# Kernel optimization log

Hardware: AMD Instinct MI355X
Metric: run time of the kernel (lower is better)

## Reference

```python
import jax, jax.numpy as jnp
import numpy as np
import math

B, D, S, H = 4, 1024, 2048, 16


def setup_inputs() -> dict:
    key = jax.random.key(0)
    ks = jax.random.split(key, 9)
    scale = 0.02
    return {
        "x": jax.random.normal(ks[0], (B, D, S), dtype=jnp.float32),
        "Wq": jax.random.normal(ks[1], (D, D), dtype=jnp.float32) * scale,
        "bq": jnp.zeros((D,), dtype=jnp.float32),
        "Wk": jax.random.normal(ks[2], (D, D), dtype=jnp.float32) * scale,
        "bk": jnp.zeros((D,), dtype=jnp.float32),
        "Wv": jax.random.normal(ks[3], (D, D), dtype=jnp.float32) * scale,
        "bv": jnp.zeros((D,), dtype=jnp.float32),
        "Wo": jax.random.normal(ks[4], (D, D), dtype=jnp.float32) * scale,
        "bo": jnp.zeros((D,), dtype=jnp.float32),
        "num_heads": H,
    }


def _positional_encoding(d_model, seq_len):
    # pe[0::2, :] = sin(pos * denom), pe[1::2, :] = cos(pos * denom)
    pos = jnp.arange(seq_len, dtype=jnp.float32)[None, :]            # [1, S]
    denom = jnp.exp(jnp.arange(0, d_model, 2, dtype=jnp.float32)
                    * (-math.log(10000.0) / d_model))[:, None]        # [D/2, 1]
    angles = pos * denom                                              # [D/2, S]
    pe = jnp.zeros((d_model, seq_len), dtype=jnp.float32)
    pe = pe.at[0::2, :].set(jnp.sin(angles))
    pe = pe.at[1::2, :].set(jnp.cos(angles))
    return pe


def reference(x, Wq, bq, Wk, bk, Wv, bv, Wo, bo, num_heads):
    b, d_model, s = x.shape
    head_dim = d_model // num_heads
    x = x + _positional_encoding(d_model, s)[None, :, :]  # broadcast over batch
    x = jnp.transpose(x, (0, 2, 1))                       # [B, S, D]
    q = x @ Wq.T + bq
    k = x @ Wk.T + bk
    v = x @ Wv.T + bv
    # [B, S, H, hd] -> [B, H, S, hd]
    q = q.reshape(b, s, num_heads, head_dim).transpose(0, 2, 1, 3)
    k = k.reshape(b, s, num_heads, head_dim).transpose(0, 2, 1, 3)
    v = v.reshape(b, s, num_heads, head_dim).transpose(0, 2, 1, 3)
    scores = jnp.einsum('bhqd,bhkd->bhqk', q, k) / jnp.sqrt(
        jnp.asarray(head_dim, dtype=jnp.float32))
    attn = jax.nn.softmax(scores, axis=-1)
    out = jnp.einsum('bhqk,bhkd->bhqd', attn, v)          # [B, H, S, hd]
    out = out.transpose(0, 2, 1, 3).reshape(b, s, d_model)
    out = out @ Wo.T + bo
    return jnp.transpose(out, (0, 2, 1))                  # [B, D, S]
```

## Files before the change

kernel.cpp:

```cpp
#include <hip/hip_runtime.h>


typedef __bf16 bf16;
typedef __attribute__((ext_vector_type(8))) __bf16 bf16x8;
typedef __attribute__((ext_vector_type(4))) __bf16 bf16x4;
typedef __attribute__((ext_vector_type(2))) __bf16 bf16x2;
typedef __attribute__((ext_vector_type(4))) float f32x4;
typedef __attribute__((ext_vector_type(2))) unsigned int uintx2;
typedef __attribute__((ext_vector_type(4))) unsigned int uintx4;

#define NB 4
#define ND 1024
#define NS 2048
#define NH 16
#define NM 8192

__device__ __forceinline__ void gld16(const void* g, void* l) {
  __builtin_amdgcn_global_load_lds((__attribute__((address_space(1))) void*)g,
                                   (__attribute__((address_space(3))) void*)l, 16, 0, 0);
}

__device__ __forceinline__ float exp2_fast(float x) {
#if __has_builtin(__builtin_amdgcn_exp2f)
  return __builtin_amdgcn_exp2f(x);
#else
  return exp2f(x);
#endif
}

__device__ __forceinline__ unsigned pk2(float a, float b) {
  bf16x2 t;
  t[0] = (bf16)a;
  t[1] = (bf16)b;
  return __builtin_bit_cast(unsigned int, t);
}

__device__ __forceinline__ void lane_xchg(unsigned a, unsigned b, unsigned& lo,
                                          unsigned& hi) {
#if __has_builtin(__builtin_amdgcn_permlane32_swap) && \
    __has_builtin(__builtin_amdgcn_permlane16_swap)
  uintx2 r = __builtin_amdgcn_permlane32_swap(a, b, false, false);
  uintx2 r2 = __builtin_amdgcn_permlane16_swap(r[0], r[1], false, false);
  lo = r2[0];
  hi = r2[1];
#else
  const int lane = threadIdx.x & 63;
  const int src = (lane & 15) + ((lane >> 4) & 1) * 32;
  const unsigned as = (unsigned)__shfl((int)a, src, 64);
  const unsigned bs = (unsigned)__shfl((int)b, src, 64);
  const unsigned as2 = (unsigned)__shfl((int)a, src + 16, 64);
  const unsigned bs2 = (unsigned)__shfl((int)b, src + 16, 64);
  lo = (lane >= 32) ? bs : as;
  hi = (lane >= 32) ? bs2 : as2;
#endif
}

__global__ __launch_bounds__(256) void prep_kernel(
    const float* __restrict__ x, const float* __restrict__ Wq,
    const float* __restrict__ Wk, const float* __restrict__ Wv,
    const float* __restrict__ Wo, bf16* __restrict__ xT, bf16* __restrict__ Wqkv,
    bf16* __restrict__ WoB) {
  const int tx = threadIdx.x, ty = threadIdx.y;
  if (blockIdx.z == NB) {
    const size_t flat = ((size_t)blockIdx.y * 64 + blockIdx.x) * 256 + ty * 32 + tx;
#pragma unroll
    for (int c = 0; c < 2; ++c) {
      const size_t i = (flat * 2 + c) * 4;
      const float* src;
      bf16* dst;
      size_t off;
      if (i < (size_t)3 * 1024 * 1024) {
        const int sel = (int)(i >> 20);
        src = sel == 0 ? Wq : (sel == 1 ? Wk : Wv);
        off = i - ((size_t)sel << 20);
        dst = Wqkv + i;
      } else {
        src = Wo;
        off = i - ((size_t)3 << 20);
        dst = WoB + off;
      }
      const f32x4 v = *(const f32x4*)(src + off);
      bf16x4 o;
      o[0] = (bf16)v[0];
      o[1] = (bf16)v[1];
      o[2] = (bf16)v[2];
      o[3] = (bf16)v[3];
      *(bf16x4*)dst = o;
    }
    return;
  }
  __shared__ float t[32][33];
  const int s0 = blockIdx.x * 32, d0 = blockIdx.y * 32, b = blockIdx.z;
#pragma unroll
  for (int i = 0; i < 4; ++i) {
    const int rr = ty + i * 8;
    const int d = d0 + rr, s = s0 + tx;
    const float freq = __expf(-(float)(d >> 1) * 0.01798894603980689f);
    const float ang = (float)s * freq;
    const float pe = (d & 1) ? __cosf(ang) : __sinf(ang);
    t[rr][tx] = x[((size_t)b * ND + d) * NS + s] + pe;
  }
  __syncthreads();
#pragma unroll
  for (int i = 0; i < 4; ++i) {
    const int a = ty + i * 8;
    xT[((size_t)b * NS + s0 + a) * ND + d0 + tx] = (bf16)t[tx][a];
  }
}

__device__ __forceinline__ void gemm_tile_128(const bf16* __restrict__ A,
                                              const bf16* __restrict__ Bm,
                                              int tm, int tn, bf16* ldsA, bf16* ldsB,
                                              f32x4 acc[4][4]) {
  const int tid = threadIdx.x;
  const int lane = tid & 63, wave = tid >> 6;
  const int wm = wave >> 1, wn = wave & 1;
  const int rl = lane & 15, quad = lane >> 4;
  int r0[4], c0[4];
#pragma unroll
  for (int j = 0; j < 4; ++j) {
    const int o = (wave * 4 + j) * 1024 + lane * 16;
    const int r = o >> 7;
    r0[j] = r;
    c0[j] = ((((o >> 4) & 7) ^ (r & 7)) * 8);
  }
  for (int kt = 0; kt < 1024; kt += 64) {
#pragma unroll
    for (int j = 0; j < 4; ++j) {
      gld16(A + (size_t)(tm + r0[j]) * 1024 + kt + c0[j], (char*)ldsA + (wave * 4 + j) * 1024);
      gld16(Bm + (size_t)(tn + r0[j]) * 1024 + kt + c0[j], (char*)ldsB + (wave * 4 + j) * 1024);
    }
    __syncthreads();
#pragma unroll
    for (int kk = 0; kk < 2; ++kk) {
      bf16x8 af[4], bfr[4];
#pragma unroll
      for (int i = 0; i < 4; ++i) {
        const int ra = wm * 64 + i * 16 + rl;
        af[i] = *(const bf16x8*)((const char*)ldsA + ra * 128 +
                                 (((kk * 4 + quad) ^ (rl & 7)) * 16));
        const int rb = wn * 64 + i * 16 + rl;
        bfr[i] = *(const bf16x8*)((const char*)ldsB + rb * 128 +
                                  (((kk * 4 + quad) ^ (rl & 7)) * 16));
      }
#pragma unroll
      for (int i = 0; i < 4; ++i)
#pragma unroll
        for (int j = 0; j < 4; ++j)
          acc[i][j] =
              __builtin_amdgcn_mfma_f32_16x16x32_bf16(af[i], bfr[j], acc[i][j], 0, 0, 0);
    }
    __syncthreads();
  }
}

__global__ __launch_bounds__(256, 3) void gemm_qkv_kernel(
    const bf16* __restrict__ xT, const bf16* __restrict__ Wqkv,
    const float* __restrict__ bq, const float* __restrict__ bk,
    const float* __restrict__ bv, bf16* __restrict__ Q, bf16* __restrict__ Kb,
    bf16* __restrict__ VT) {
  __shared__ bf16 ldsA[128 * 64], ldsB[128 * 64];
  const int tm = blockIdx.x * 128, tn = blockIdx.y * 128;
  f32x4 acc[4][4];
  const f32x4 z = {0.f, 0.f, 0.f, 0.f};
#pragma unroll
  for (int i = 0; i < 4; ++i)
#pragma unroll
    for (int j = 0; j < 4; ++j) acc[i][j] = z;
  gemm_tile_128(xT, Wqkv, tm, tn, ldsA, ldsB, acc);
  const int lane = threadIdx.x & 63, wave = threadIdx.x >> 6;
  const int wm = wave >> 1, wn = wave & 1;
  const int rl = lane & 15, quad = lane >> 4;
  const float QSCALE = 0.18033688011112042f;
#pragma unroll
  for (int j = 0; j < 4; ++j) {
    const int n = tn + wn * 64 + j * 16 + rl;
    const int which = n >> 10;
    const int nl = n & 1023;
    const int h = nl >> 6, d = nl & 63;
    const float bias = (which == 0 ? bq : which == 1 ? bk : bv)[nl];
#pragma unroll
    for (int i = 0; i < 4; ++i) {
      const int m0 = tm + wm * 64 + i * 16 + quad * 4;
      const int b = m0 >> 11, s0 = m0 & 2047;
      const size_t bh = (size_t)(b * 16 + h);
      if (which == 2) {
        bf16x4 pk;
#pragma unroll
        for (int r = 0; r < 4; ++r) pk[r] = (bf16)(acc[i][j][r] + bias);
        *(bf16x4*)(VT + ((size_t)bh * 64 + d) * 2048 + s0) = pk;
      } else {
#pragma unroll
        for (int r = 0; r < 4; ++r) {
          const float v = acc[i][j][r] + bias;
          const int s = s0 + r;
          if (which == 0)
            Q[(bh * 2048 + s) * 64 + d] = (bf16)(v * QSCALE);
          else
            Kb[(bh * 2048 + s) * 64 + d] = (bf16)v;
        }
      }
    }
  }
}

__global__ __launch_bounds__(256, 4) void attn_kernel(const bf16* __restrict__ Q,
                                                      const bf16* __restrict__ Kb,
                                                      const bf16* __restrict__ VT,
                                                      bf16* __restrict__ AO) {
  __shared__ __align__(16) char smem[32768];
  char* ldsK = smem;
  char* ldsV = smem + 16384;
  const int tid = threadIdx.x;
  const int lane = tid & 63, wave = tid >> 6;
  const int rl = lane & 15, quad = lane >> 4;
  const int bh = blockIdx.x;
  const int q0 = blockIdx.y * 128;
  const bf16* Qb = Q + ((size_t)bh * 2048 + q0) * 64;
  const bf16* Kbb = Kb + (size_t)bh * 2048 * 64;
  const bf16* Vb = VT + (size_t)bh * 64 * 2048;
  const int o0 = wave * 1024 + lane * 16, o1 = o0 + 4096;
  const int ra = o0 >> 7, rb = o1 >> 7;
  const int ca = (((o0 >> 4) & 7) ^ (ra & 7)) * 16;
  const int cb = (((o1 >> 4) & 7) ^ (rb & 7)) * 16;
  gld16((const char*)Kbb + (size_t)ra * 128 + ca, ldsK + wave * 1024);
  gld16((const char*)Kbb + (size_t)rb * 128 + cb, ldsK + wave * 1024 + 4096);
  gld16((const char*)Vb + (size_t)ra * 4096 + ca, ldsV + wave * 1024);
  gld16((const char*)Vb + (size_t)rb * 4096 + cb, ldsV + wave * 1024 + 4096);
  bf16x8 qf[2][2];
#pragma unroll
  for (int i = 0; i < 2; ++i)
#pragma unroll
    for (int ks = 0; ks < 2; ++ks)
      qf[i][ks] =
          *(const bf16x8*)(Qb + (wave * 32 + i * 16 + rl) * 64 + ks * 32 + quad * 8);
  f32x4 o_acc[2][4], lacc[2];
  const f32x4 z = {0.f, 0.f, 0.f, 0.f};
#pragma unroll
  for (int i = 0; i < 2; ++i) {
    lacc[i] = z;
#pragma unroll
    for (int j = 0; j < 4; ++j) o_acc[i][j] = z;
  }
  const bf16 oneb = (bf16)1.0f;
  const bf16x8 onesb = {oneb, oneb, oneb, oneb, oneb, oneb, oneb, oneb};
  int buf = 0;
  for (int kt = 0; kt < 2048; kt += 64, buf ^= 1) {
    __syncthreads();
    if (kt + 64 < 2048) {
      const int nb = (buf ^ 1) * 8192;
      gld16((const char*)Kbb + (size_t)(kt + 64 + ra) * 128 + ca, ldsK + nb + wave * 1024);
      gld16((const char*)Kbb + (size_t)(kt + 64 + rb) * 128 + cb,
            ldsK + nb + wave * 1024 + 4096);
      gld16((const char*)Vb + (size_t)ra * 4096 + (size_t)(kt + 64) * 2 + ca,
            ldsV + nb + wave * 1024);
      gld16((const char*)Vb + (size_t)rb * 4096 + (size_t)(kt + 64) * 2 + cb,
            ldsV + nb + wave * 1024 + 4096);
    }
    const char* Kbase = ldsK + buf * 8192;
    const char* Vbase = ldsV + buf * 8192;
#pragma unroll
    for (int ks = 0; ks < 2; ++ks) {
      const int jk0 = ks * 2, jk1 = ks * 2 + 1;
      const bf16x8 k00 =
          *(const bf16x8*)(Kbase + (jk0 * 16 + rl) * 128 + ((quad ^ (rl & 7)) * 16));
      const bf16x8 k01 =
          *(const bf16x8*)(Kbase + (jk0 * 16 + rl) * 128 + (((4 + quad) ^ (rl & 7)) * 16));
      const bf16x8 k10 =
          *(const bf16x8*)(Kbase + (jk1 * 16 + rl) * 128 + ((quad ^ (rl & 7)) * 16));
      const bf16x8 k11 =
          *(const bf16x8*)(Kbase + (jk1 * 16 + rl) * 128 + (((4 + quad) ^ (rl & 7)) * 16));
      bf16x8 pf[2];
#pragma unroll
      for (int i = 0; i < 2; ++i) {
        f32x4 s0 = z, s1 = z;
        s0 = __builtin_amdgcn_mfma_f32_16x16x32_bf16(k00, qf[i][0], s0, 0, 0, 0);
        s0 = __builtin_amdgcn_mfma_f32_16x16x32_bf16(k01, qf[i][1], s0, 0, 0, 0);
        s1 = __builtin_amdgcn_mfma_f32_16x16x32_bf16(k10, qf[i][0], s1, 0, 0, 0);
        s1 = __builtin_amdgcn_mfma_f32_16x16x32_bf16(k11, qf[i][1], s1, 0, 0, 0);
        const unsigned a0 = pk2(exp2_fast(s0[0]), exp2_fast(s0[1]));
        const unsigned a1 = pk2(exp2_fast(s0[2]), exp2_fast(s0[3]));
        const unsigned b0 = pk2(exp2_fast(s1[0]), exp2_fast(s1[1]));
        const unsigned b1 = pk2(exp2_fast(s1[2]), exp2_fast(s1[3]));
        unsigned d0, d1, d2, d3;
        lane_xchg(a0, b0, d0, d2);
        lane_xchg(a1, b1, d1, d3);
        uintx4 dd;
        dd[0] = d0;
        dd[1] = d1;
        dd[2] = d2;
        dd[3] = d3;
        pf[i] = __builtin_bit_cast(bf16x8, dd);
        lacc[i] =
            __builtin_amdgcn_mfma_f32_16x16x32_bf16(pf[i], onesb, lacc[i], 0, 0, 0);
      }
#pragma unroll
      for (int j = 0; j < 4; ++j) {
        const bf16x8 vf = *(const bf16x8*)(Vbase + (j * 16 + rl) * 128 +
                                           (((ks * 4 + quad) ^ (rl & 7)) * 16));
#pragma unroll
        for (int i = 0; i < 2; ++i)
          o_acc[i][j] =
              __builtin_amdgcn_mfma_f32_16x16x32_bf16(pf[i], vf, o_acc[i][j], 0, 0, 0);
      }
    }
  }
  const int b = bh >> 4, h = bh & 15;
#pragma unroll
  for (int i = 0; i < 2; ++i) {
    f32x4 linv;
#pragma unroll
    for (int r = 0; r < 4; ++r) linv[r] = __builtin_amdgcn_rcpf(lacc[i][r]);
#pragma unroll
    for (int j = 0; j < 4; ++j)
#pragma unroll
      for (int r = 0; r < 4; ++r) {
        const int s = q0 + wave * 32 + i * 16 + quad * 4 + r;
        const int d = h * 64 + j * 16 + rl;
        AO[((size_t)b * 2048 + s) * 1024 + d] = (bf16)(o_acc[i][j][r] * linv[r]);
      }
  }
}

__global__ __launch_bounds__(256, 3) void gemm_out_kernel(const bf16* __restrict__ AO,
                                                          const bf16* __restrict__ WoB,
                                                          const float* __restrict__ bo,
                                                          float* __restrict__ out) {
  __shared__ bf16 ldsA[128 * 64], ldsB[128 * 64];
  const int tm = blockIdx.x * 128, tn = blockIdx.y * 128;
  f32x4 acc[4][4];
  const f32x4 z = {0.f, 0.f, 0.f, 0.f};
#pragma unroll
  for (int i = 0; i < 4; ++i)
#pragma unroll
    for (int j = 0; j < 4; ++j) acc[i][j] = z;
  gemm_tile_128(AO, WoB, tm, tn, ldsA, ldsB, acc);
  const int lane = threadIdx.x & 63, wave = threadIdx.x >> 6;
  const int wm = wave >> 1, wn = wave & 1;
  const int rl = lane & 15, quad = lane >> 4;
#pragma unroll
  for (int j = 0; j < 4; ++j) {
    const int n = tn + wn * 64 + j * 16 + rl;
    const float bias = bo[n];
#pragma unroll
    for (int i = 0; i < 4; ++i) {
      const int m0 = tm + wm * 64 + i * 16 + quad * 4;
      const int b = m0 >> 11, s = m0 & 2047;
      f32x4 v = acc[i][j];
      v[0] += bias;
      v[1] += bias;
      v[2] += bias;
      v[3] += bias;
      *(f32x4*)(out + ((size_t)(b * 1024 + n)) * 2048 + s) = v;
    }
  }
}

extern "C" void kernel_launch(void* const* d_in, const int* in_sizes, int n_in,
                              void* d_out, int out_size, void* d_ws, size_t ws_size,
                              hipStream_t stream) {
  const float* x = (const float*)d_in[0];
  const float* Wq = (const float*)d_in[1];
  const float* bq = (const float*)d_in[2];
  const float* Wk = (const float*)d_in[3];
  const float* bk = (const float*)d_in[4];
  const float* Wv = (const float*)d_in[5];
  const float* bv = (const float*)d_in[6];
  const float* Wo = (const float*)d_in[7];
  const float* bo = (const float*)d_in[8];
  float* out = (float*)d_out;

  char* p = (char*)d_ws;
  bf16* xT = (bf16*)p;
  p += (size_t)NM * ND * 2;
  bf16* Wqkv = (bf16*)p;
  p += (size_t)3 * ND * ND * 2;
  bf16* WoB = (bf16*)p;
  p += (size_t)ND * ND * 2;
  bf16* Qb = (bf16*)p;
  p += (size_t)NM * ND * 2;
  bf16* Kbf = (bf16*)p;
  p += (size_t)NM * ND * 2;
  bf16* VTb = (bf16*)p;
  p += (size_t)NM * ND * 2;
  bf16* AO = xT;

  prep_kernel<<<dim3(NS / 32, ND / 32, NB + 1), dim3(32, 8), 0, stream>>>(
      x, Wq, Wk, Wv, Wo, xT, Wqkv, WoB);
  gemm_qkv_kernel<<<dim3(NM / 128, 3072 / 128), dim3(256), 0, stream>>>(
      xT, Wqkv, bq, bk, bv, Qb, Kbf, VTb);
  attn_kernel<<<dim3(NB * NH, NS / 128), dim3(256), 0, stream>>>(Qb, Kbf, VTb, AO);
  gemm_out_kernel<<<dim3(NM / 128, ND / 128), dim3(256), 0, stream>>>(AO, WoB, bo, out);
}
```

Baseline: 261.2 us.

## Rewrite QKV GEMM with 256x256 tiles, 8 waves and double-buffered LDS prefetch

Replaces the 128x128 QKV projection GEMM with a 512-thread kernel computing 256x256 tiles. It double-buffers 128KB of LDS, issues global-to-LDS loads for the next K-step interleaved with MFMA phases, and uses explicit waitcnt/barriers and setprio. The goal is more data reuse per tile and hiding global load latency behind compute. In exchange, large LDS use limits occupancy, the grid has only 384 blocks, and the hand-placed barriers add fragility. The out-GEMM launch bound also drops from 3 to 2 waves.

Measured after the change: 285.8 us. 1.09x slower.

```diff
diff --git a/kernel.cpp b/kernel.cpp
--- a/kernel.cpp
+++ b/kernel.cpp
@@ -108,6 +108,128 @@
   }
 }
 
+__global__ __launch_bounds__(512, 2) void gemm_qkv_kernel(
+    const bf16* __restrict__ xT, const bf16* __restrict__ Wqkv,
+    const float* __restrict__ bq, const float* __restrict__ bk,
+    const float* __restrict__ bv, bf16* __restrict__ Q, bf16* __restrict__ Kb,
+    bf16* __restrict__ VT) {
+  __shared__ __align__(16) char smem[131072];
+  char* ldsA = smem;
+  char* ldsB = smem + 65536;
+  const int tid = threadIdx.x;
+  const int lane = tid & 63, wave = tid >> 6;
+  const int wm = wave >> 2, wn = wave & 3;
+  const int rl = lane & 15, quad = lane >> 4;
+  const int tm = blockIdx.x * 256, tn = blockIdx.y * 256;
+  int row[4], colv[4];
+#pragma unroll
+  for (int g = 0; g < 4; ++g) {
+    const int c = g * 512 + tid;
+    const int r = c >> 3;
+    row[g] = r;
+    colv[g] = (((c & 7) ^ (r & 7)) * 8);
+  }
+  f32x4 acc[8][4];
+  const f32x4 z = {0.f, 0.f, 0.f, 0.f};
+#pragma unroll
+  for (int i = 0; i < 8; ++i)
+#pragma unroll
+    for (int j = 0; j < 4; ++j) acc[i][j] = z;
+#pragma unroll
+  for (int g = 0; g < 4; ++g) {
+    gld16(xT + (size_t)(tm + row[g]) * 1024 + colv[g], ldsA + g * 8192 + tid * 16);
+    gld16(Wqkv + (size_t)(tn + row[g]) * 1024 + colv[g], ldsB + g * 8192 + tid * 16);
+  }
+  for (int t = 0; t < 16; ++t) {
+    const int cur = t & 1;
+    const char* Ab = ldsA + cur * 32768;
+    const char* Bb = ldsB + cur * 32768;
+    const int nb = (cur ^ 1) * 32768;
+    const int ktn = (t + 1) * 64;
+#pragma unroll
+    for (int p = 0; p < 4; ++p) {
+      if (p == 0) {
+        if (t < 15) {
+          gld16(xT + (size_t)(tm + row[0]) * 1024 + ktn + colv[0],
+                ldsA + nb + tid * 16);
+          gld16(Wqkv + (size_t)(tn + row[0]) * 1024 + ktn + colv[0],
+                ldsB + nb + tid * 16);
+          asm volatile("s_waitcnt vmcnt(2)" ::: "memory");
+        } else {
+          asm volatile("s_waitcnt vmcnt(0)" ::: "memory");
+        }
+        asm volatile("s_barrier" ::: "memory");
+      }
+      const int mq = p >> 1, nq = p & 1;
+      bf16x8 af[4][2], bfr[2][2];
+#pragma unroll
+      for (int i = 0; i < 4; ++i) {
+        const int ra = wm * 128 + mq * 64 + i * 16 + rl;
+#pragma unroll
+        for (int kk = 0; kk < 2; ++kk)
+          af[i][kk] =
+              *(const bf16x8*)(Ab + ra * 128 + (((kk * 4 + quad) ^ (rl & 7)) * 16));
+      }
+#pragma unroll
+      for (int j = 0; j < 2; ++j) {
+        const int rb = wn * 64 + nq * 32 + j * 16 + rl;
+#pragma unroll
+        for (int kk = 0; kk < 2; ++kk)
+          bfr[j][kk] =
+              *(const bf16x8*)(Bb + rb * 128 + (((kk * 4 + quad) ^ (rl & 7)) * 16));
+      }
+      if (p != 0 && t < 15) {
+        gld16(xT + (size_t)(tm + row[p]) * 1024 + ktn + colv[p],
+              ldsA + nb + p * 8192 + tid * 16);
+        gld16(Wqkv + (size_t)(tn + row[p]) * 1024 + ktn + colv[p],
+              ldsB + nb + p * 8192 + tid * 16);
+      }
+      if (p != 0) asm volatile("s_barrier" ::: "memory");
+      __builtin_amdgcn_s_setprio(1);
+#pragma unroll
+      for (int kk = 0; kk < 2; ++kk)
+#pragma unroll
+        for (int i = 0; i < 4; ++i)
+#pragma unroll
+          for (int j = 0; j < 2; ++j)
+            acc[mq * 4 + i][nq * 2 + j] = __builtin_amdgcn_mfma_f32_16x16x32_bf16(
+                af[i][kk], bfr[j][kk], acc[mq * 4 + i][nq * 2 + j], 0, 0, 0);
+      __builtin_amdgcn_s_setprio(0);
+      asm volatile("s_barrier" ::: "memory");
+    }
+  }
+  const float QSCALE = 0.18033688011112042f;
+#pragma unroll
+  for (int nj = 0; nj < 4; ++nj) {
+    const int n = tn + wn * 64 + nj * 16 + rl;
+    const int which = n >> 10;
+    const int nl = n & 1023;
+    const int h = nl >> 6, d = nl & 63;
+    const float bias = (which == 0 ? bq : which == 1 ? bk : bv)[nl];
+#pragma unroll
+    for (int mi = 0; mi < 8; ++mi) {
+      const int m0 = tm + wm * 128 + mi * 16 + quad * 4;
+      const int b = m0 >> 11, s0 = m0 & 2047;
+      const size_t bh = (size_t)(b * 16 + h);
+      const f32x4 a = acc[mi][nj];
+      if (which == 2) {
+        bf16x4 pk;
+#pragma unroll
+        for (int r = 0; r < 4; ++r) pk[r] = (bf16)(a[r] + bias);
+        *(bf16x4*)(VT + ((size_t)bh * 64 + d) * 2048 + s0) = pk;
+      } else if (which == 0) {
+#pragma unroll
+        for (int r = 0; r < 4; ++r)
+          Q[(bh * 2048 + s0 + r) * 64 + d] = (bf16)((a[r] + bias) * QSCALE);
+      } else {
+#pragma unroll
+        for (int r = 0; r < 4; ++r)
+          Kb[(bh * 2048 + s0 + r) * 64 + d] = (bf16)(a[r] + bias);
+      }
+    }
+  }
+}
+
 __device__ __forceinline__ void gemm_tile_128(const bf16* __restrict__ A,
                                               const bf16* __restrict__ Bm,
                                               int tm, int tn, bf16* ldsA, bf16* ldsB,
@@ -151,56 +273,6 @@
               __builtin_amdgcn_mfma_f32_16x16x32_bf16(af[i], bfr[j], acc[i][j], 0, 0, 0);
     }
     __syncthreads();
-  }
-}
-
-__global__ __launch_bounds__(256, 3) void gemm_qkv_kernel(
-    const bf16* __restrict__ xT, const bf16* __restrict__ Wqkv,
-    const float* __restrict__ bq, const float* __restrict__ bk,
-    const float* __restrict__ bv, bf16* __restrict__ Q, bf16* __restrict__ Kb,
-    bf16* __restrict__ VT) {
-  __shared__ bf16 ldsA[128 * 64], ldsB[128 * 64];
-  const int tm = blockIdx.x * 128, tn = blockIdx.y * 128;
-  f32x4 acc[4][4];
-  const f32x4 z = {0.f, 0.f, 0.f, 0.f};
-#pragma unroll
-  for (int i = 0; i < 4; ++i)
-#pragma unroll
-    for (int j = 0; j < 4; ++j) acc[i][j] = z;
-  gemm_tile_128(xT, Wqkv, tm, tn, ldsA, ldsB, acc);
-  const int lane = threadIdx.x & 63, wave = threadIdx.x >> 6;
-  const int wm = wave >> 1, wn = wave & 1;
-  const int rl = lane & 15, quad = lane >> 4;
-  const float QSCALE = 0.18033688011112042f;
-#pragma unroll
-  for (int j = 0; j < 4; ++j) {
-    const int n = tn + wn * 64 + j * 16 + rl;
-    const int which = n >> 10;
-    const int nl = n & 1023;
-    const int h = nl >> 6, d = nl & 63;
-    const float bias = (which == 0 ? bq : which == 1 ? bk : bv)[nl];
-#pragma unroll
-    for (int i = 0; i < 4; ++i) {
-      const int m0 = tm + wm * 64 + i * 16 + quad * 4;
-      const int b = m0 >> 11, s0 = m0 & 2047;
-      const size_t bh = (size_t)(b * 16 + h);
-      if (which == 2) {
-        bf16x4 pk;
-#pragma unroll
-        for (int r = 0; r < 4; ++r) pk[r] = (bf16)(acc[i][j][r] + bias);
-        *(bf16x4*)(VT + ((size_t)bh * 64 + d) * 2048 + s0) = pk;
-      } else {
-#pragma unroll
-        for (int r = 0; r < 4; ++r) {
-          const float v = acc[i][j][r] + bias;
-          const int s = s0 + r;
-          if (which == 0)
-            Q[(bh * 2048 + s) * 64 + d] = (bf16)(v * QSCALE);
-          else
-            Kb[(bh * 2048 + s) * 64 + d] = (bf16)v;
-        }
-      }
-    }
   }
 }
 
@@ -322,7 +394,7 @@
   }
 }
 
-__global__ __launch_bounds__(256, 3) void gemm_out_kernel(const bf16* __restrict__ AO,
+__global__ __launch_bounds__(256, 2) void gemm_out_kernel(const bf16* __restrict__ AO,
                                                           const bf16* __restrict__ WoB,
                                                           const float* __restrict__ bo,
                                                           float* __restrict__ out) {
@@ -387,7 +459,7 @@
 
   prep_kernel<<<dim3(NS / 32, ND / 32, NB + 1), dim3(32, 8), 0, stream>>>(
       x, Wq, Wk, Wv, Wo, xT, Wqkv, WoB);
-  gemm_qkv_kernel<<<dim3(NM / 128, 3072 / 128), dim3(256), 0, stream>>>(
+  gemm_qkv_kernel<<<dim3(NM / 256, 3072 / 256), dim3(512), 0, stream>>>(
       xT, Wqkv, bq, bk, bv, Qb, Kbf, VTb);
   attn_kernel<<<dim3(NB * NH, NS / 128), dim3(256), 0, stream>>>(Qb, Kbf, VTb, AO);
   gemm_out_kernel<<<dim3(NM / 128, ND / 128), dim3(256), 0, stream>>>(AO, WoB, bo, out);
```
